# Kernel optimization log

Hardware: AMD Instinct MI355X
Metric: run time of the kernel (lower is better)

Reference implementation:

```python
import jax, jax.numpy as jnp
import numpy as np

B, N, D, K = 16, 512, 64, 8  # batch, num_nodes, node_dim, num_edge_class


def setup_inputs() -> dict:
    key = jax.random.key(0)
    ks = jax.random.split(key, 6)
    return {
        "node_states": jax.random.normal(ks[0], (B, N, D), jnp.float32),
        "adjacency_in": jax.random.randint(ks[1], (B, N, N), 0, K + 1, jnp.int32),
        "distance": jax.random.normal(ks[2], (B, N, N), jnp.float32),  # declared but unused, as in source
        "matrices_in": jax.random.normal(ks[3], (K, D, D), jnp.float32) * 0.1,
        "matrices_out": jax.random.normal(ks[4], (K, D, D), jnp.float32) * 0.1,
        "message_bias": jax.random.normal(ks[5], (2 * D,), jnp.float32) * 0.1,
    }


def reference(node_states, adjacency_in, distance, matrices_in, matrices_out, message_bias):
    # node_states: [B, N, D]; adjacency_in: [B, N, N] int in [0, K]; 0 = no edge.
    node_dim = node_states.shape[-1]
    zeros = jnp.zeros((1, node_dim, node_dim), node_states.dtype)
    Min = jnp.concatenate([zeros, matrices_in], axis=0)    # [K+1, D, D]
    Mout = jnp.concatenate([zeros, matrices_out], axis=0)  # [K+1, D, D]
    # Transform every node state by every edge-type matrix once:
    # T[b, j, k, d] = sum_e M[k, d, e] * h[b, j, e]
    T_in = jnp.einsum('kde,bje->bjkd', Min, node_states)
    T_out = jnp.einsum('kde,bje->bjkd', Mout, node_states)
    # One-hot edge types: oh[b, i, j, k] = [adjacency_in[b, i, j] == k]
    oh = jax.nn.one_hot(adjacency_in, Min.shape[0], dtype=node_states.dtype)  # [B, N, N, K+1]
    # a_in_mul[b, i, d]  = sum_j M_in[adj[b,i,j]]  @ h[b, j]  (identical math to the
    # dense [B, N*D, N*D] block-matmul in the TF source, without materializing it)
    a_in_mul = jnp.einsum('bijk,bjkd->bid', oh, T_in)
    # a_out uses the transposed adjacency: adj_out[b,i,j] = adj[b,j,i]
    a_out_mul = jnp.einsum('bjik,bjkd->bid', oh, T_out)
    messages = jnp.concatenate([a_in_mul, a_out_mul], axis=-1) + message_bias
    return messages  # [B, N, 2*D]
```

## Files before the change

kernel.cpp:

```cpp
#include <hip/hip_runtime.h>
#include <hip/hip_fp16.h>

#define B_ 16
#define N_ 512
#define D_ 64
#define K_ 8

#define WSU_BYTES ((size_t)B_ * N_ * N_ * 4)
#define T_BYTES   ((size_t)B_ * N_ * (K_ + 1) * D_ * 2)
#define TROWB 1152
#define TOUT_OFF (T_BYTES / 2)

typedef __attribute__((ext_vector_type(8))) short bf8_t;
typedef __attribute__((ext_vector_type(4))) float f4_t;

__device__ __forceinline__ unsigned short f2bf(float x) {
  union { float f; unsigned u; } c; c.f = x;
  unsigned r = c.u + 0x7FFFu + ((c.u >> 16) & 1u);
  return (unsigned short)(r >> 16);
}

__device__ __forceinline__ bf8_t pack_bf8(const float* p) {
  const float4 a = *(const float4*)p;
  const float4 b = *(const float4*)(p + 4);
  union { unsigned u[4]; bf8_t v; } r;
  r.u[0] = (unsigned)f2bf(a.x) | ((unsigned)f2bf(a.y) << 16);
  r.u[1] = (unsigned)f2bf(a.z) | ((unsigned)f2bf(a.w) << 16);
  r.u[2] = (unsigned)f2bf(b.x) | ((unsigned)f2bf(b.y) << 16);
  r.u[3] = (unsigned)f2bf(b.z) | ((unsigned)f2bf(b.w) << 16);
  return r.v;
}

__global__ __launch_bounds__(256) void prep_adj(const int* __restrict__ adj,
                                                unsigned* __restrict__ wsu) {
  __shared__ int ta[64][65];
  __shared__ int tb[64][65];
  const int blk = blockIdx.x;
  const int xcd = blk & 7, rest = blk >> 3;
  const int b = xcd + 8 * (rest & 1);
  const int tile = rest >> 1;
  const int i0 = (tile >> 3) * 64, j0 = (tile & 7) * 64;
  const int lane = threadIdx.x & 63, w = threadIdx.x >> 6;
  const int* ab = adj + (size_t)b * N_ * N_;
#pragma unroll
  for (int r = w; r < 64; r += 4) {
    ta[r][lane] = ab[(size_t)(i0 + r) * N_ + j0 + lane];
    tb[r][lane] = ab[(size_t)(j0 + r) * N_ + i0 + lane];
  }
  __syncthreads();
  unsigned* wb = wsu + (size_t)b * N_ * N_;
#pragma unroll
  for (int r = w; r < 64; r += 4) {
    wb[(size_t)(i0 + r) * N_ + j0 + lane] =
        (unsigned)(ta[r][lane] << 7) | ((unsigned)tb[lane][r] << 23);
  }
}

__global__ __launch_bounds__(256) void build_T_mfma(
    const float* __restrict__ h,
    const float* __restrict__ Min,
    const float* __restrict__ Mout,
    unsigned short* __restrict__ Tin) {
  const int blk = blockIdx.x;
  const int b   = (blk & 7) + 8 * ((blk >> 3) & 1);
  const int u   = blk >> 4;
  const int kdt = u >> 3;
  const int jt4 = u & 7;
  const int w = threadIdx.x >> 6, l = threadIdx.x & 63;
  const int j0  = (jt4 * 4 + w) * 16;
  const int kd0 = kdt * 64;
  const int r16 = l & 15, grp = l >> 4;

  const float* hrp = h + ((size_t)(b * N_ + j0 + r16)) * 64 + grp * 8;
  bf8_t hfr[2];
  hfr[0] = pack_bf8(hrp);
  hfr[1] = pack_bf8(hrp + 32);

  const float* Mbase = (kd0 >= 512) ? Mout : Min;
  const float* mrp = Mbase + (size_t)((kd0 & 511) + r16) * 64 + grp * 8;

  f4_t acc[4];
#pragma unroll
  for (int fc = 0; fc < 4; ++fc) acc[fc] = (f4_t)(0.f);
#pragma unroll
  for (int fc = 0; fc < 4; ++fc) {
    const bf8_t a0 = pack_bf8(mrp + (size_t)fc * 16 * 64);
    const bf8_t a1 = pack_bf8(mrp + (size_t)fc * 16 * 64 + 32);
    acc[fc] = __builtin_amdgcn_mfma_f32_16x16x32_bf16(a0, hfr[0], acc[fc], 0, 0, 0);
    acc[fc] = __builtin_amdgcn_mfma_f32_16x16x32_bf16(a1, hfr[1], acc[fc], 0, 0, 0);
  }

  unsigned short* Tb = Tin + ((kd0 >= 512) ? TOUT_OFF : 0) + (size_t)b * N_ * 576;
  const int kdl = kd0 & 511;
  const int j = j0 + r16;
  unsigned short* trow = Tb + (size_t)j * 576 + 64 + kdl + grp * 4;
#pragma unroll
  for (int fc = 0; fc < 4; ++fc) {
    const __half2 lo = __floats2half2_rn(acc[fc][0], acc[fc][1]);
    const __half2 hi = __floats2half2_rn(acc[fc][2], acc[fc][3]);
    uint2 pk;
    pk.x = *(const unsigned*)&lo;
    pk.y = *(const unsigned*)&hi;
    *(uint2*)(trow + fc * 16) = pk;
  }

  if (kdt == 0) {
    unsigned short* s0 = Tin + (size_t)b * N_ * 576 + (size_t)j * 576 + grp * 16;
    const int4 z = make_int4(0, 0, 0, 0);
    *(int4*)(s0)                 = z;
    *(int4*)(s0 + 8)             = z;
    *(int4*)(s0 + TOUT_OFF)      = z;
    *(int4*)(s0 + TOUT_OFF + 8)  = z;
  }
}

__global__ __launch_bounds__(512, 8) void gather_msg(
    const unsigned* __restrict__ wsu,
    const unsigned short* __restrict__ Tin,
    const float* __restrict__ bias,
    float* __restrict__ out) {
  __shared__ unsigned ed[8 * 512];
  const int blk = blockIdx.x;
  const int b  = (blk & 7) + 8 * ((blk >> 3) & 1);
  const int rb = blk >> 4;
  const int tid = threadIdx.x;
  const int w = tid >> 6, lane = tid & 63;
  const int wq = w & 3, jh = w >> 2;
  const int half = lane >> 5, lane5 = lane & 31;
  const int dir = lane5 >> 4;
  const int dl  = lane5 & 15;
  const int row_l = wq * 2 + half;

  {
    const int4* src = (const int4*)(wsu + ((size_t)(b * N_ + rb * 8)) * N_);
    int4* dst = (int4*)ed;
    dst[tid]       = src[tid];
    dst[tid + 512] = src[tid + 512];
  }
  __syncthreads();

  const unsigned* edrow = ed + row_l * 512 + jh * 256;
  const unsigned shr_ = (unsigned)dir * 16u;
  const char* base = (const char*)Tin + (size_t)b * N_ * TROWB;
  unsigned vb = (unsigned)jh * 256u * (unsigned)TROWB +
                (unsigned)dir * (unsigned)T_BYTES + (unsigned)dl * 8u;

  float fa0 = 0.f, fa1 = 0.f, fa2 = 0.f, fa3 = 0.f;
  for (int jw = 0; jw < 4; ++jw) {
    __half2 a0 = __floats2half2_rn(0.f, 0.f);
    __half2 a1 = __floats2half2_rn(0.f, 0.f);
#pragma unroll
    for (int j4 = 0; j4 < 16; ++j4) {
      const uint4 ew = *(const uint4*)(edrow + jw * 64 + j4 * 4);
#pragma unroll
      for (int t = 0; t < 4; ++t) {
        const unsigned wvv = (t == 0) ? ew.x : (t == 1) ? ew.y : (t == 2) ? ew.z : ew.w;
        const unsigned off = (wvv >> shr_) & 0xFFFFu;
        const uint2 u = *(const uint2*)(base + (vb + off));
        a0 = __hadd2(a0, *(const __half2*)&u.x);
        a1 = __hadd2(a1, *(const __half2*)&u.y);
        vb += TROWB;
      }
    }
    const float2 f0 = __half22float2(a0);
    const float2 f1 = __half22float2(a1);
    fa0 += f0.x; fa1 += f0.y; fa2 += f1.x; fa3 += f1.y;
  }

  __syncthreads();
  float4* pbuf = (float4*)ed;
  if (jh == 1) pbuf[wq * 64 + lane] = make_float4(fa0, fa1, fa2, fa3);
  __syncthreads();
  if (jh == 0) {
    const float4 p = pbuf[wq * 64 + lane];
    const int row = rb * 8 + row_l;
    const int d0 = dl * 4;
    float4 r;
    r.x = fa0 + p.x + bias[dir * 64 + d0];
    r.y = fa1 + p.y + bias[dir * 64 + d0 + 1];
    r.z = fa2 + p.z + bias[dir * 64 + d0 + 2];
    r.w = fa3 + p.w + bias[dir * 64 + d0 + 3];
    *(float4*)(out + ((size_t)b * N_ + row) * (2 * D_) + dir * 64 + d0) = r;
  }
}

#define ACCUM(kv, bucket) switch (kv) { \
    case 1: (bucket)[0] += v_; break; case 2: (bucket)[1] += v_; break; \
    case 3: (bucket)[2] += v_; break; case 4: (bucket)[3] += v_; break; \
    case 5: (bucket)[4] += v_; break; case 6: (bucket)[5] += v_; break; \
    case 7: (bucket)[6] += v_; break; case 8: (bucket)[7] += v_; break; \
    default: break; }

__global__ __launch_bounds__(64) void ggnn_fallback(
    const float* __restrict__ h, const int* __restrict__ adj,
    const float* __restrict__ Min, const float* __restrict__ Mout,
    const float* __restrict__ bias, float* __restrict__ out) {
  const int blk = blockIdx.x;
  const int b  = blk / (N_ / 2);
  const int i0 = (blk % (N_ / 2)) * 2;
  const int d  = threadIdx.x;
  float s_in[2][K_], s_out[2][K_];
#pragma unroll
  for (int r = 0; r < 2; ++r)
#pragma unroll
    for (int k = 0; k < K_; ++k) { s_in[r][k] = 0.f; s_out[r][k] = 0.f; }
  const int* rowp0 = adj + (b * N_ + i0) * N_;
  const int* rowp1 = rowp0 + N_;
  const int* colp  = adj + b * N_ * N_ + i0;
  const float* hb  = h + b * N_ * D_ + d;
  for (int j0 = 0; j0 < N_; j0 += 8) {
    float hv[8]; int kr0[8], kr1[8], kc0[8], kc1[8];
#pragma unroll
    for (int m = 0; m < 8; ++m) {
      hv[m] = hb[(j0 + m) * D_];
      kr0[m] = rowp0[j0 + m]; kr1[m] = rowp1[j0 + m];
      kc0[m] = colp[(j0 + m) * N_]; kc1[m] = colp[(j0 + m) * N_ + 1];
    }
#pragma unroll
    for (int m = 0; m < 8; ++m) {
      const float v_ = hv[m];
      ACCUM(kr0[m], s_in[0]); ACCUM(kr1[m], s_in[1]);
      ACCUM(kc0[m], s_out[0]); ACCUM(kc1[m], s_out[1]);
    }
  }
  __shared__ float S[2][2][K_][D_];
#pragma unroll
  for (int r = 0; r < 2; ++r)
#pragma unroll
    for (int k = 0; k < K_; ++k) { S[r][0][k][d] = s_in[r][k]; S[r][1][k][d] = s_out[r][k]; }
  __syncthreads();
  float acc_in[2], acc_out[2];
#pragma unroll
  for (int r = 0; r < 2; ++r) { acc_in[r] = bias[d]; acc_out[r] = bias[D_ + d]; }
  for (int k = 0; k < K_; ++k) {
#pragma unroll
    for (int e0 = 0; e0 < D_; e0 += 4) {
      const float4 mi = *(const float4*)(Min  + (k * D_ + d) * D_ + e0);
      const float4 mo = *(const float4*)(Mout + (k * D_ + d) * D_ + e0);
#pragma unroll
      for (int r = 0; r < 2; ++r) {
        const float4 si = *(const float4*)(&S[r][0][k][e0]);
        const float4 so = *(const float4*)(&S[r][1][k][e0]);
        acc_in[r]  += mi.x * si.x + mi.y * si.y + mi.z * si.z + mi.w * si.w;
        acc_out[r] += mo.x * so.x + mo.y * so.y + mo.z * so.z + mo.w * so.w;
      }
    }
  }
#pragma unroll
  for (int r = 0; r < 2; ++r) {
    out[(b * N_ + i0 + r) * (2 * D_) + d]      = acc_in[r];
    out[(b * N_ + i0 + r) * (2 * D_) + D_ + d] = acc_out[r];
  }
}

extern "C" void kernel_launch(void* const* d_in, const int* in_sizes, int n_in,
                              void* d_out, int out_size, void* d_ws, size_t ws_size,
                              hipStream_t stream) {
  const float* h    = (const float*)d_in[0];
  const int*   adj  = (const int*)d_in[1];
  const float* Min  = (const float*)d_in[3];
  const float* Mout = (const float*)d_in[4];
  const float* bias = (const float*)d_in[5];
  float* out = (float*)d_out;

  if (ws_size < WSU_BYTES + 2 * T_BYTES) {
    hipLaunchKernelGGL(ggnn_fallback, dim3(B_ * N_ / 2), dim3(64), 0, stream,
                       h, adj, Min, Mout, bias, out);
    return;
  }
  unsigned*       wsu = (unsigned*)d_ws;
  unsigned short* Tin = (unsigned short*)((char*)d_ws + WSU_BYTES);

  hipLaunchKernelGGL(prep_adj,     dim3(1024), dim3(256), 0, stream, adj, wsu);
  hipLaunchKernelGGL(build_T_mfma, dim3(2048), dim3(256), 0, stream, h, Min, Mout, Tin);
  hipLaunchKernelGGL(gather_msg,   dim3(1024), dim3(512), 0, stream, wsu, Tin, bias, out);
}
```

Baseline: 171.9 us.

## Fuse adjacency transpose into gather kernel with double-buffered LDS windows

Removes the separate prep_adj pass, which wrote a packed 16 MB in/out edge-type workspace. The gather kernel now reads adjacency tiles directly and transposes them through shared memory. It double-buffers 64-column windows, prefetching the next window while accumulating the current one. Each block now covers 16 rows with all 8 warps, so the grid halves and the cross-warp reduction disappears. The trade-offs are a barrier per window and strided transposed reads of adj columns.

```diff
diff --git a/kernel.cpp b/kernel.cpp
--- a/kernel.cpp
+++ b/kernel.cpp
@@ -6,7 +6,6 @@
 #define D_ 64
 #define K_ 8
 
-#define WSU_BYTES ((size_t)B_ * N_ * N_ * 4)
 #define T_BYTES   ((size_t)B_ * N_ * (K_ + 1) * D_ * 2)
 #define TROWB 1152
 #define TOUT_OFF (T_BYTES / 2)
@@ -29,31 +28,6 @@
   r.u[2] = (unsigned)f2bf(b.x) | ((unsigned)f2bf(b.y) << 16);
   r.u[3] = (unsigned)f2bf(b.z) | ((unsigned)f2bf(b.w) << 16);
   return r.v;
-}
-
-__global__ __launch_bounds__(256) void prep_adj(const int* __restrict__ adj,
-                                                unsigned* __restrict__ wsu) {
-  __shared__ int ta[64][65];
-  __shared__ int tb[64][65];
-  const int blk = blockIdx.x;
-  const int xcd = blk & 7, rest = blk >> 3;
-  const int b = xcd + 8 * (rest & 1);
-  const int tile = rest >> 1;
-  const int i0 = (tile >> 3) * 64, j0 = (tile & 7) * 64;
-  const int lane = threadIdx.x & 63, w = threadIdx.x >> 6;
-  const int* ab = adj + (size_t)b * N_ * N_;
-#pragma unroll
-  for (int r = w; r < 64; r += 4) {
-    ta[r][lane] = ab[(size_t)(i0 + r) * N_ + j0 + lane];
-    tb[r][lane] = ab[(size_t)(j0 + r) * N_ + i0 + lane];
-  }
-  __syncthreads();
-  unsigned* wb = wsu + (size_t)b * N_ * N_;
-#pragma unroll
-  for (int r = w; r < 64; r += 4) {
-    wb[(size_t)(i0 + r) * N_ + j0 + lane] =
-        (unsigned)(ta[r][lane] << 7) | ((unsigned)tb[lane][r] << 23);
-  }
 }
 
 __global__ __launch_bounds__(256) void build_T_mfma(
@@ -114,49 +88,70 @@
   }
 }
 
-__global__ __launch_bounds__(512, 8) void gather_msg(
-    const unsigned* __restrict__ wsu,
+__global__ __launch_bounds__(512, 4) void gather_fused(
+    const int* __restrict__ adj,
     const unsigned short* __restrict__ Tin,
     const float* __restrict__ bias,
     float* __restrict__ out) {
-  __shared__ unsigned ed[8 * 512];
+  __shared__ int ed [2][16][72];
+  __shared__ int edT[2][16][72];
   const int blk = blockIdx.x;
   const int b  = (blk & 7) + 8 * ((blk >> 3) & 1);
   const int rb = blk >> 4;
+  const int i0 = rb * 16;
   const int tid = threadIdx.x;
   const int w = tid >> 6, lane = tid & 63;
-  const int wq = w & 3, jh = w >> 2;
   const int half = lane >> 5, lane5 = lane & 31;
   const int dir = lane5 >> 4;
   const int dl  = lane5 & 15;
-  const int row_l = wq * 2 + half;
-
-  {
-    const int4* src = (const int4*)(wsu + ((size_t)(b * N_ + rb * 8)) * N_);
-    int4* dst = (int4*)ed;
-    dst[tid]       = src[tid];
-    dst[tid + 512] = src[tid + 512];
+  const int row_l = w * 2 + half;
+
+  const int* adjb = adj + (size_t)b * N_ * N_;
+
+  const bool s_kin = (tid < 256);
+  const int sr  = tid >> 4, sc4 = (tid & 15) * 4;
+  const int t2  = tid & 255;
+  const int sjr = t2 >> 2, sc = (t2 & 3) * 4;
+
+  if (s_kin) {
+    const int4 v = *(const int4*)(adjb + (size_t)(i0 + sr) * N_ + sc4);
+    *(int4*)&ed[0][sr][sc4] = v;
+  } else {
+    const int4 v = *(const int4*)(adjb + (size_t)sjr * N_ + i0 + sc);
+    edT[0][sc][sjr] = v.x; edT[0][sc + 1][sjr] = v.y;
+    edT[0][sc + 2][sjr] = v.z; edT[0][sc + 3][sjr] = v.w;
   }
   __syncthreads();
 
-  const unsigned* edrow = ed + row_l * 512 + jh * 256;
-  const unsigned shr_ = (unsigned)dir * 16u;
-  const char* base = (const char*)Tin + (size_t)b * N_ * TROWB;
-  unsigned vb = (unsigned)jh * 256u * (unsigned)TROWB +
-                (unsigned)dir * (unsigned)T_BYTES + (unsigned)dl * 8u;
-
+  const char* tbase = (const char*)Tin + (size_t)b * N_ * TROWB;
+  unsigned vb = (unsigned)dir * (unsigned)T_BYTES + (unsigned)dl * 8u;
   float fa0 = 0.f, fa1 = 0.f, fa2 = 0.f, fa3 = 0.f;
-  for (int jw = 0; jw < 4; ++jw) {
+  int buf = 0;
+
+  for (int win = 0; win < 8; ++win) {
+    if (win < 7) {
+      const int j0n = (win + 1) * 64;
+      if (s_kin) {
+        const int4 v = *(const int4*)(adjb + (size_t)(i0 + sr) * N_ + j0n + sc4);
+        *(int4*)&ed[buf ^ 1][sr][sc4] = v;
+      } else {
+        const int4 v = *(const int4*)(adjb + (size_t)(j0n + sjr) * N_ + i0 + sc);
+        edT[buf ^ 1][sc][sjr] = v.x; edT[buf ^ 1][sc + 1][sjr] = v.y;
+        edT[buf ^ 1][sc + 2][sjr] = v.z; edT[buf ^ 1][sc + 3][sjr] = v.w;
+      }
+    }
+
+    const int* krow = dir ? &edT[buf][row_l][0] : &ed[buf][row_l][0];
     __half2 a0 = __floats2half2_rn(0.f, 0.f);
     __half2 a1 = __floats2half2_rn(0.f, 0.f);
 #pragma unroll
     for (int j4 = 0; j4 < 16; ++j4) {
-      const uint4 ew = *(const uint4*)(edrow + jw * 64 + j4 * 4);
+      const int4 kv4 = *(const int4*)&krow[j4 * 4];
 #pragma unroll
       for (int t = 0; t < 4; ++t) {
-        const unsigned wvv = (t == 0) ? ew.x : (t == 1) ? ew.y : (t == 2) ? ew.z : ew.w;
-        const unsigned off = (wvv >> shr_) & 0xFFFFu;
-        const uint2 u = *(const uint2*)(base + (vb + off));
+        const unsigned kv = (unsigned)((t == 0) ? kv4.x : (t == 1) ? kv4.y
+                                      : (t == 2) ? kv4.z : kv4.w);
+        const uint2 u = *(const uint2*)(tbase + (vb + (kv << 7)));
         a0 = __hadd2(a0, *(const __half2*)&u.x);
         a1 = __hadd2(a1, *(const __half2*)&u.y);
         vb += TROWB;
@@ -165,23 +160,19 @@
     const float2 f0 = __half22float2(a0);
     const float2 f1 = __half22float2(a1);
     fa0 += f0.x; fa1 += f0.y; fa2 += f1.x; fa3 += f1.y;
-  }
-
-  __syncthreads();
-  float4* pbuf = (float4*)ed;
-  if (jh == 1) pbuf[wq * 64 + lane] = make_float4(fa0, fa1, fa2, fa3);
-  __syncthreads();
-  if (jh == 0) {
-    const float4 p = pbuf[wq * 64 + lane];
-    const int row = rb * 8 + row_l;
-    const int d0 = dl * 4;
-    float4 r;
-    r.x = fa0 + p.x + bias[dir * 64 + d0];
-    r.y = fa1 + p.y + bias[dir * 64 + d0 + 1];
-    r.z = fa2 + p.z + bias[dir * 64 + d0 + 2];
-    r.w = fa3 + p.w + bias[dir * 64 + d0 + 3];
-    *(float4*)(out + ((size_t)b * N_ + row) * (2 * D_) + dir * 64 + d0) = r;
-  }
+
+    __syncthreads();
+    buf ^= 1;
+  }
+
+  const int row = i0 + row_l;
+  const int d0 = dl * 4;
+  float4 r;
+  r.x = fa0 + bias[dir * 64 + d0];
+  r.y = fa1 + bias[dir * 64 + d0 + 1];
+  r.z = fa2 + bias[dir * 64 + d0 + 2];
+  r.w = fa3 + bias[dir * 64 + d0 + 3];
+  *(float4*)(out + ((size_t)b * N_ + row) * (2 * D_) + dir * 64 + d0) = r;
 }
 
 #define ACCUM(kv, bucket) switch (kv) { \
@@ -263,15 +254,13 @@
   const float* bias = (const float*)d_in[5];
   float* out = (float*)d_out;
 
-  if (ws_size < WSU_BYTES + 2 * T_BYTES) {
+  if (ws_size < 2 * T_BYTES) {
     hipLaunchKernelGGL(ggnn_fallback, dim3(B_ * N_ / 2), dim3(64), 0, stream,
                        h, adj, Min, Mout, bias, out);
     return;
   }
-  unsigned*       wsu = (unsigned*)d_ws;
-  unsigned short* Tin = (unsigned short*)((char*)d_ws + WSU_BYTES);
-
-  hipLaunchKernelGGL(prep_adj,     dim3(1024), dim3(256), 0, stream, adj, wsu);
+  unsigned short* Tin = (unsigned short*)d_ws;
+
   hipLaunchKernelGGL(build_T_mfma, dim3(2048), dim3(256), 0, stream, h, Min, Mout, Tin);
-  hipLaunchKernelGGL(gather_msg,   dim3(1024), dim3(512), 0, stream, wsu, Tin, bias, out);
-}
+  hipLaunchKernelGGL(gather_fused, dim3(512),  dim3(512), 0, stream, adj, Tin, bias, out);
+}
```

Result: faster. 166.7 us (-3.0%).
